# Kernel tuning notes

Hardware: AMD Instinct MI355X
Metric: run time of the kernel (lower is better)

The kernel has to match this reference:

```python
import jax, jax.numpy as jnp
import numpy as np

# Scene / model dims (match init_kwargs)
H, W, T = 128, 128, 8
N = 1024  # number of 3D (x,y,t) Gaussians, layer 0

CHOL_BOUND_3D = jnp.array([0.5, 0.0, 0.5, 0.5, 0.0, 0.5], dtype=jnp.float32)


def setup_inputs() -> dict:
    key = jax.random.key(0)
    k1, k2, k3 = jax.random.split(key, 3)
    xyz = jax.random.normal(k1, (N, 3), dtype=jnp.float32)          # raw (pre-tanh) positions
    cholesky = jax.random.uniform(k2, (N, 6), dtype=jnp.float32)    # raw cholesky params
    cholesky = cholesky.at[:, 5].add(float(T))                      # _init_layer0: data[:,5] += T
    features = jax.random.uniform(k3, (N, 3), dtype=jnp.float32)    # rgb features
    opacity = jnp.ones((N, 1), dtype=jnp.float32)                   # layer-0 opacity buffer (ones)
    background = jnp.ones((3,), dtype=jnp.float32)                  # unused by the sum-rasterizer
    return {"xyz": xyz, "cholesky": cholesky, "features": features,
            "opacity": opacity, "background": background}


def _render(xyz, cholesky, features, opacity):
    # --- project_gaussians_video ---
    # positions: tanh -> ndc (-1,1) -> pixel/frame coords (ndc2pix: 0.5*((v+1)*S - 1))
    sizes = jnp.array([W, H, T], dtype=jnp.float32)
    means = 0.5 * ((jnp.tanh(xyz) + 1.0) * sizes - 1.0)             # (N,3) in (x,y,t)
    c = cholesky + CHOL_BOUND_3D                                     # get_cholesky_elements
    # lower-triangular L, column-major packing: [L00,L10,L20,L11,L21,L22]
    L = jnp.zeros((N, 3, 3), dtype=c.dtype)
    L = L.at[:, 0, 0].set(c[:, 0]).at[:, 1, 0].set(c[:, 1]).at[:, 2, 0].set(c[:, 2])
    L = L.at[:, 1, 1].set(c[:, 3]).at[:, 2, 1].set(c[:, 4]).at[:, 2, 2].set(c[:, 5])
    cov = jnp.einsum('nij,nkj->nik', L, L)                           # Sigma = L L^T
    conic = jnp.linalg.inv(cov)                                      # (N,3,3), symmetric

    # --- rasterize_gaussians_sum_video (dense reference, no tile culling) ---
    # sigma(p) = 0.5 p^T Q p - p^T Q m + 0.5 m^T Q m, expressed as a [P,10] x [10,N] matmul
    qm = jnp.einsum('nij,nj->ni', conic, means)                      # (N,3)
    const = 0.5 * jnp.einsum('ni,ni->n', means, qm)                  # (N,)
    G = jnp.stack([0.5 * conic[:, 0, 0], 0.5 * conic[:, 1, 1], 0.5 * conic[:, 2, 2],
                   conic[:, 0, 1], conic[:, 0, 2], conic[:, 1, 2],
                   -qm[:, 0], -qm[:, 1], -qm[:, 2], const], axis=1)  # (N,10)

    ts = jnp.arange(T, dtype=jnp.float32)
    ys = jnp.arange(H, dtype=jnp.float32)
    xs = jnp.arange(W, dtype=jnp.float32)
    pt, py, px = jnp.meshgrid(ts, ys, xs, indexing='ij')             # (T,H,W) — t-major pixel order
    px, py, pt = px.ravel(), py.ravel(), pt.ravel()                  # (P,), P = T*H*W
    F = jnp.stack([px * px, py * py, pt * pt, px * py, px * pt, py * pt,
                   px, py, pt, jnp.ones_like(px)], axis=1)           # (P,10)

    sigma = F @ G.T                                                  # (P,N) — memory-bound hot loop
    wgt = jnp.exp(-sigma) * opacity[:, 0][None, :]                   # alpha per pixel/gaussian
    img = wgt @ features                                             # (P,3) alpha-weighted sum blend
    img = jnp.clip(img, 0.0, 1.0)
    # view(-1,T,H,W,3).permute(0,4,2,3,1) -> (1,3,H,W,T)
    return jnp.transpose(img.reshape(1, T, H, W, 3), (0, 4, 2, 3, 1))


def reference(xyz, cholesky, features, opacity, background):
    return _render(xyz, cholesky, features, opacity)
```

## Files before the change

kernel.cpp:

```cpp
#include <hip/hip_runtime.h>
#include <math.h>

#define HH 128
#define WW 128
#define TT 8
#define NG 1024
#define PP (HH * WW * TT)

__device__ __forceinline__ float fast_tanh(float x) {
    float e = __builtin_amdgcn_exp2f(x * 2.885390081777926814f);
    return 1.f - 2.f * __builtin_amdgcn_rcpf(e + 1.f);
}

__global__ __launch_bounds__(256) void gv_fused(
    const float* __restrict__ xyz,
    const float* __restrict__ chol,
    const float* __restrict__ feat,
    const float* __restrict__ opac,
    float* __restrict__ out)
{
    __shared__ __align__(16) float recs[NG * 8];
    __shared__ int sidx[NG];
    __shared__ int cnt_lds[4];

    const int tid = threadIdx.x;
    const int lane = tid & 63;
    const int wv = tid >> 6;
    const int r0 = blockIdx.x * 2;
    const float y0f = (float)(r0 & 127);
    const float tf  = (float)(r0 >> 7);
    const float kneg = -1.44269504088896340736f;

    {
        int cnt = 0;
#pragma unroll
        for (int it = 0; it < 4; ++it) {
            const int n = wv * 256 + it * 64 + lane;
            float vy = xyz[n * 3 + 1];
            float c1 = chol[n * 6 + 1];
            float c3 = chol[n * 6 + 3] + 0.5f;
            float my = fmaf(fast_tanh(vy), 64.f, 63.5f);
            float syy = fmaf(c1, c1, c3 * c3);
            float d0 = my - y0f;
            float d1 = d0 - 1.f;
            float dmin = fminf(fabsf(d0), fabsf(d1));
            bool keep = dmin * dmin < 32.f * syy;

            unsigned long long mask = __ballot(keep);
            if (keep) {
                int pos = __builtin_amdgcn_mbcnt_hi(
                              (unsigned)(mask >> 32),
                              __builtin_amdgcn_mbcnt_lo((unsigned)mask, 0));
                sidx[wv * 256 + cnt + pos] = n;
            }
            cnt += (int)__popcll(mask);
        }
        if (lane == 0) cnt_lds[wv] = cnt;
    }
    __syncthreads();

    const int c0s = cnt_lds[0], c1s = cnt_lds[1];
    const int c2s = cnt_lds[2], c3s = cnt_lds[3];
    const int off1 = c0s, off2 = c0s + c1s, off3 = c0s + c1s + c2s;
    const int S = off3 + c3s;

    for (int j = tid; j < S; j += 256) {
        int seg = (j >= off1) + (j >= off2) + (j >= off3);
        int base = seg == 0 ? 0 : (seg == 1 ? off1 : (seg == 2 ? off2 : off3));
        const int n = sidx[seg * 256 + (j - base)];

        float vx = xyz[n * 3 + 0], vy = xyz[n * 3 + 1], vt = xyz[n * 3 + 2];
        float mx = 0.5f * ((fast_tanh(vx) + 1.f) * (float)WW - 1.f);
        float my = 0.5f * ((fast_tanh(vy) + 1.f) * (float)HH - 1.f);
        float mt = 0.5f * ((fast_tanh(vt) + 1.f) * (float)TT - 1.f);

        float c0 = chol[n * 6 + 0] + 0.5f;
        float c1 = chol[n * 6 + 1];
        float c2 = chol[n * 6 + 2] + 0.5f;
        float c3 = chol[n * 6 + 3] + 0.5f;
        float c4 = chol[n * 6 + 4];
        float c5 = chol[n * 6 + 5] + 0.5f;

        float a  = c0 * c0;
        float b  = c0 * c1;
        float cc = c0 * c2;
        float d  = c1 * c1 + c3 * c3;
        float e  = c1 * c2 + c3 * c4;
        float f  = c2 * c2 + c4 * c4 + c5 * c5;

        float A00 = d * f - e * e;
        float A01 = cc * e - b * f;
        float A02 = b * e - cc * d;
        float A11 = a * f - cc * cc;
        float A12 = b * cc - a * e;
        float A22 = a * d - b * b;
        float det = a * A00 + b * A01 + cc * A02;
        float rdet = 1.f / det;
        float Q00 = A00 * rdet, Q01 = A01 * rdet, Q02 = A02 * rdet;
        float Q11 = A11 * rdet, Q12 = A12 * rdet, Q22 = A22 * rdet;

        float qmx = Q00 * mx + Q01 * my + Q02 * mt;
        float qmy = Q01 * mx + Q11 * my + Q12 * mt;
        float qmt = Q02 * mx + Q12 * my + Q22 * mt;
        float cst = 0.5f * (mx * qmx + my * qmy + mt * qmt);

        float G0 = 0.5f * Q00, G1 = 0.5f * Q11, G2 = 0.5f * Q22;
        float G3 = Q01, G4 = Q02, G5 = Q12;
        float G6 = -qmx, G7 = -qmy, G8 = -qmt, G9 = cst;

        float u  = fmaf(G4, tf, G6);
        float v  = fmaf(G5, tf, G7);
        float w0 = fmaf(fmaf(G2, tf, G8), tf, G9);
        float B0 = fmaf(G3, y0f, u);
        float C0 = fmaf(fmaf(G1, y0f, v), y0f, w0);
        float y1f = y0f + 1.f;
        float B1 = fmaf(G3, y1f, u);
        float C1 = fmaf(fmaf(G1, y1f, v), y1f, w0);

        float op = opac[n];
        float4* l4 = (float4*)recs;
        l4[j * 2 + 0] = (float4){kneg * G0, op * feat[n * 3 + 0],
                                 op * feat[n * 3 + 1], op * feat[n * 3 + 2]};
        l4[j * 2 + 1] = (float4){kneg * B0, kneg * C0, kneg * B1, kneg * C1};
    }
    __syncthreads();

    const int rowi = wv >> 1;
    const int x = (wv & 1) * 64 + lane;
    const float xf = (float)x;
    float a0 = 0.f, a1 = 0.f, a2 = 0.f;
    const float4* lds4 = (const float4*)recs;

#pragma unroll 4
    for (int m = 0; m < S; ++m) {
        float4 af = lds4[m * 2];
        float2 bc = *(const float2*)&recs[m * 8 + 4 + 2 * rowi];
        float s = fmaf(fmaf(af.x, xf, bc.x), xf, bc.y);
        float w = __builtin_amdgcn_exp2f(s);
        a0 = fmaf(w, af.y, a0);
        a1 = fmaf(w, af.z, a1);
        a2 = fmaf(w, af.w, a2);
    }

    a0 = fminf(fmaxf(a0, 0.f), 1.f);
    a1 = fminf(fmaxf(a1, 0.f), 1.f);
    a2 = fminf(fmaxf(a2, 0.f), 1.f);

    const int r = r0 + rowi;
    const int y = r & 127, t = r >> 7;
    const int base_o = (y * WW + x) * TT + t;
    out[base_o] = a0;
    out[base_o + PP] = a1;
    out[base_o + 2 * PP] = a2;
}

extern "C" void kernel_launch(void* const* d_in, const int* in_sizes, int n_in,
                              void* d_out, int out_size, void* d_ws, size_t ws_size,
                              hipStream_t stream) {
    const float* xyz  = (const float*)d_in[0];
    const float* chol = (const float*)d_in[1];
    const float* feat = (const float*)d_in[2];
    const float* opac = (const float*)d_in[3];
    float* out = (float*)d_out;

    const int blocks = (TT * HH) / 2;
    gv_fused<<<blocks, 256, 0, stream>>>(xyz, chol, feat, opac, out);
}
```

Before: 13.29 us.

## Split Gaussian list across two half-blocks and reduce partial sums in LDS

Doubles the block to 512 threads. The two halves each cull and preprocess half of the Gaussians, then accumulate pixel sums over their half, and the partial sums are combined through shared memory before the write. This halves the serial per-pixel loop length and per-thread setup, which is meant to cut latency in a launch of only 512 blocks. In exchange it adds an extra barrier, an LDS reduction, and idle threads in one half during the output write.

Result: faster. 12.59 us (median of 2 runs) (-5.2%).

```diff
diff --git a/kernel.cpp b/kernel.cpp
--- a/kernel.cpp
+++ b/kernel.cpp
@@ -6,26 +6,30 @@
 #define TT 8
 #define NG 1024
 #define PP (HH * WW * TT)
+#define GH 512
 
 __device__ __forceinline__ float fast_tanh(float x) {
     float e = __builtin_amdgcn_exp2f(x * 2.885390081777926814f);
     return 1.f - 2.f * __builtin_amdgcn_rcpf(e + 1.f);
 }
 
-__global__ __launch_bounds__(256) void gv_fused(
+__global__ __launch_bounds__(512) void gv_fused(
     const float* __restrict__ xyz,
     const float* __restrict__ chol,
     const float* __restrict__ feat,
     const float* __restrict__ opac,
     float* __restrict__ out)
 {
-    __shared__ __align__(16) float recs[NG * 8];
-    __shared__ int sidx[NG];
-    __shared__ int cnt_lds[4];
+    __shared__ __align__(16) float recs[2][GH * 8];
+    __shared__ int sidx[2][GH];
+    __shared__ int cnt_lds[8];
+    __shared__ float pbuf[4][3][64];
 
     const int tid = threadIdx.x;
     const int lane = tid & 63;
     const int wv = tid >> 6;
+    const int h = wv >> 2;
+    const int seg_i = wv & 3;
     const int r0 = blockIdx.x * 2;
     const float y0f = (float)(r0 & 127);
     const float tf  = (float)(r0 >> 7);
@@ -34,8 +38,8 @@
     {
         int cnt = 0;
 #pragma unroll
-        for (int it = 0; it < 4; ++it) {
-            const int n = wv * 256 + it * 64 + lane;
+        for (int it = 0; it < 2; ++it) {
+            const int n = h * GH + seg_i * 128 + it * 64 + lane;
             float vy = xyz[n * 3 + 1];
             float c1 = chol[n * 6 + 1];
             float c3 = chol[n * 6 + 3] + 0.5f;
@@ -51,7 +55,7 @@
                 int pos = __builtin_amdgcn_mbcnt_hi(
                               (unsigned)(mask >> 32),
                               __builtin_amdgcn_mbcnt_lo((unsigned)mask, 0));
-                sidx[wv * 256 + cnt + pos] = n;
+                sidx[h][seg_i * 128 + cnt + pos] = n;
             }
             cnt += (int)__popcll(mask);
         }
@@ -59,15 +63,16 @@
     }
     __syncthreads();
 
-    const int c0s = cnt_lds[0], c1s = cnt_lds[1];
-    const int c2s = cnt_lds[2], c3s = cnt_lds[3];
-    const int off1 = c0s, off2 = c0s + c1s, off3 = c0s + c1s + c2s;
-    const int S = off3 + c3s;
+    const int b0 = cnt_lds[h * 4 + 0], b1 = cnt_lds[h * 4 + 1];
+    const int b2 = cnt_lds[h * 4 + 2], b3 = cnt_lds[h * 4 + 3];
+    const int off1 = b0, off2 = b0 + b1, off3 = b0 + b1 + b2;
+    const int S = off3 + b3;
 
-    for (int j = tid; j < S; j += 256) {
+    const int tg = tid & 255;
+    for (int j = tg; j < S; j += 256) {
         int seg = (j >= off1) + (j >= off2) + (j >= off3);
         int base = seg == 0 ? 0 : (seg == 1 ? off1 : (seg == 2 ? off2 : off3));
-        const int n = sidx[seg * 256 + (j - base)];
+        const int n = sidx[h][seg * 128 + (j - base)];
 
         float vx = xyz[n * 3 + 0], vy = xyz[n * 3 + 1], vt = xyz[n * 3 + 2];
         float mx = 0.5f * ((fast_tanh(vx) + 1.f) * (float)WW - 1.f);
@@ -118,23 +123,25 @@
         float C1 = fmaf(fmaf(G1, y1f, v), y1f, w0);
 
         float op = opac[n];
-        float4* l4 = (float4*)recs;
+        float4* l4 = (float4*)recs[h];
         l4[j * 2 + 0] = (float4){kneg * G0, op * feat[n * 3 + 0],
                                  op * feat[n * 3 + 1], op * feat[n * 3 + 2]};
         l4[j * 2 + 1] = (float4){kneg * B0, kneg * C0, kneg * B1, kneg * C1};
     }
     __syncthreads();
 
-    const int rowi = wv >> 1;
-    const int x = (wv & 1) * 64 + lane;
+    const int combo = wv & 3;
+    const int rowi = combo >> 1;
+    const int x = (combo & 1) * 64 + lane;
     const float xf = (float)x;
     float a0 = 0.f, a1 = 0.f, a2 = 0.f;
-    const float4* lds4 = (const float4*)recs;
+    const float4* lds4 = (const float4*)recs[h];
+    const float* recf = recs[h];
 
 #pragma unroll 4
     for (int m = 0; m < S; ++m) {
         float4 af = lds4[m * 2];
-        float2 bc = *(const float2*)&recs[m * 8 + 4 + 2 * rowi];
+        float2 bc = *(const float2*)&recf[m * 8 + 4 + 2 * rowi];
         float s = fmaf(fmaf(af.x, xf, bc.x), xf, bc.y);
         float w = __builtin_amdgcn_exp2f(s);
         a0 = fmaf(w, af.y, a0);
@@ -142,16 +149,29 @@
         a2 = fmaf(w, af.w, a2);
     }
 
-    a0 = fminf(fmaxf(a0, 0.f), 1.f);
-    a1 = fminf(fmaxf(a1, 0.f), 1.f);
-    a2 = fminf(fmaxf(a2, 0.f), 1.f);
+    if (h == 1) {
+        pbuf[combo][0][lane] = a0;
+        pbuf[combo][1][lane] = a1;
+        pbuf[combo][2][lane] = a2;
+    }
+    __syncthreads();
 
-    const int r = r0 + rowi;
-    const int y = r & 127, t = r >> 7;
-    const int base_o = (y * WW + x) * TT + t;
-    out[base_o] = a0;
-    out[base_o + PP] = a1;
-    out[base_o + 2 * PP] = a2;
+    if (h == 0) {
+        a0 += pbuf[combo][0][lane];
+        a1 += pbuf[combo][1][lane];
+        a2 += pbuf[combo][2][lane];
+
+        a0 = fminf(fmaxf(a0, 0.f), 1.f);
+        a1 = fminf(fmaxf(a1, 0.f), 1.f);
+        a2 = fminf(fmaxf(a2, 0.f), 1.f);
+
+        const int r = r0 + rowi;
+        const int y = r & 127, t = r >> 7;
+        const int base_o = (y * WW + x) * TT + t;
+        out[base_o] = a0;
+        out[base_o + PP] = a1;
+        out[base_o + 2 * PP] = a2;
+    }
 }
 
 extern "C" void kernel_launch(void* const* d_in, const int* in_sizes, int n_in,
@@ -164,5 +184,5 @@
     float* out = (float*)d_out;
 
     const int blocks = (TT * HH) / 2;
-    gv_fused<<<blocks, 256, 0, stream>>>(xyz, chol, feat, opac, out);
+    gv_fused<<<blocks, 512, 0, stream>>>(xyz, chol, feat, opac, out);
 }
```
